# Kernel tuning notes

Measured on AMD Instinct MI355X. Metric: run time of the kernel, lower is better.

Reference implementation:

```python
import jax, jax.numpy as jnp
import numpy as np

N, E, B, D, H, L = 50000, 800000, 16, 64, 128, 2


def _lin(h, w, b):
    return h @ w + b


def _scatter_mean(v, idx, n):
    s = jax.ops.segment_sum(v, idx, num_segments=n)
    c = jax.ops.segment_sum(jnp.ones((v.shape[0],), v.dtype), idx, num_segments=n)
    return s / jnp.maximum(c, 1.0)[:, None]


def setup_inputs() -> dict:
    key = jax.random.key(0)
    ks = iter(jax.random.split(key, 40))

    def p(*shape):
        return jax.random.normal(next(ks), shape, dtype=jnp.float32) * 0.05

    inp = {
        "x": jax.random.normal(next(ks), (N, D), dtype=jnp.float32),
        "edge_attr": jax.random.normal(next(ks), (E, D), dtype=jnp.float32),
        "u": jax.random.normal(next(ks), (B, D), dtype=jnp.float32),
        "e_w1": p(L, 4 * D, H), "e_b1": p(L, H),
        "e_w2": p(L, H, H), "e_b2": p(L, H),
        "e_w3": p(L, H, D), "e_b3": p(L, D),
        "n1_w1": p(L, 2 * D, H), "n1_b1": p(L, H),
        "n1_w2": p(L, H, H), "n1_b2": p(L, H),
        "n2_w1": p(L, D + H + D, H), "n2_b1": p(L, H),
        "n2_w2": p(L, H, D), "n2_b2": p(L, D),
        "g_w1": p(L, 3 * D, H), "g_b1": p(L, H),
        "g_w2": p(L, H, D), "g_b2": p(L, D),
        "edge_index": jax.random.randint(next(ks), (2, E), 0, N, dtype=jnp.int32),
        "batch": jnp.sort(jax.random.randint(next(ks), (N,), 0, B, dtype=jnp.int32)),
    }
    return inp


def _forward(x, edge_attr, u, params, edge_index, batch):
    row, col = edge_index[0], edge_index[1]
    eb = batch[row]  # [E] graph id per edge
    x0, e0, u0 = x, edge_attr, u
    for l in range(L):
        (e_w1, e_b1, e_w2, e_b2, e_w3, e_b3,
         n1_w1, n1_b1, n1_w2, n1_b2,
         n2_w1, n2_b1, n2_w2, n2_b2,
         g_w1, g_b1, g_w2, g_b2) = [pm[l] for pm in params]
        # Edge model: [E, e+2n+u] -> MLP -> [E, D]
        h = jnp.concatenate([x[row], x[col], edge_attr, u[eb]], axis=1)
        h = jax.nn.relu(_lin(h, e_w1, e_b1))
        h = jax.nn.relu(_lin(h, e_w2, e_b2))
        edge_attr = _lin(h, e_w3, e_b3)
        # Node model: gather src node + edge, MLP1, scatter_mean onto dest, MLP2
        se = jnp.concatenate([x[row], edge_attr], axis=1)  # [E, 2D]
        se = _lin(jax.nn.relu(_lin(se, n1_w1, n1_b1)), n1_w2, n1_b2)
        agg = _scatter_mean(se, col, N)  # [N, H]
        xh = jnp.concatenate([x, agg, u[batch]], axis=1)
        x = _lin(jax.nn.relu(_lin(xh, n2_w1, n2_b1)), n2_w2, n2_b2)
        # Global model: per-graph means of updated nodes/edges
        e_agg = _scatter_mean(edge_attr, eb, B)
        n_agg = _scatter_mean(x, batch, B)
        uh = jnp.concatenate([u, n_agg, e_agg], axis=1)
        u = _lin(jax.nn.relu(_lin(uh, g_w1, g_b1)), g_w2, g_b2)
    return x + x0, edge_attr + e0, u + u0


def reference(x, edge_attr, u, e_w1, e_b1, e_w2, e_b2, e_w3, e_b3, n1_w1, n1_b1, n1_w2, n1_b2, n2_w1, n2_b1, n2_w2, n2_b2, g_w1, g_b1, g_w2, g_b2, edge_index, batch):
    params = (e_w1, e_b1, e_w2, e_b2, e_w3, e_b3,
              n1_w1, n1_b1, n1_w2, n1_b2,
              n2_w1, n2_b1, n2_w2, n2_b2,
              g_w1, g_b1, g_w2, g_b2)
    return _forward(x, edge_attr, u, params, edge_index, batch)
```

## Files before the change

kernel.cpp:

```cpp
#include <hip/hip_runtime.h>

#define N_NODES 50000
#define E_EDGES 800000
#define NG 16
#define DD 64
#define HH 128
#define NB_SCAN 49

typedef __attribute__((ext_vector_type(8))) __bf16 bf16x8;
typedef __attribute__((ext_vector_type(4))) float f32x4;
typedef unsigned int uint;
typedef unsigned short ushort;
typedef __attribute__((ext_vector_type(4))) uint uint4v;

#define MFMA16(a,b,c) __builtin_amdgcn_mfma_f32_16x16x32_bf16((a),(b),(c),0,0,0)

__device__ __forceinline__ ushort f2bf(float f){
  uint u = __builtin_bit_cast(uint, f);
  u += 0x7fffu + ((u >> 16) & 1u);
  return (ushort)(u >> 16);
}
__device__ __forceinline__ uint pk2(float a, float b){
  return (uint)f2bf(a) | ((uint)f2bf(b) << 16);
}
__device__ __forceinline__ float bflo(uint u){ return __builtin_bit_cast(float, u << 16); }
__device__ __forceinline__ float bfhi(uint u){ return __builtin_bit_cast(float, u & 0xffff0000u); }

__device__ __forceinline__ void bar(){
  asm volatile("s_waitcnt lgkmcnt(0)" ::: "memory");
  __builtin_amdgcn_s_barrier();
}
#define VMWAIT(n) asm volatile("s_waitcnt vmcnt(" #n ")" ::: "memory")

__device__ __forceinline__ void gload16(const void* g, void* l){
  __builtin_amdgcn_global_load_lds(
      (const __attribute__((address_space(1))) unsigned int*)g,
      (__attribute__((address_space(3))) unsigned int*)l, 16, 0, 0);
}

__device__ __forceinline__ bf16x8 ldfrag(const char* base, int row, int byteoff){
  uint4v v = *(const uint4v*)(base + row*256 + (byteoff ^ ((row & 7) << 4)));
  return __builtin_bit_cast(bf16x8, v);
}
__device__ __forceinline__ uint4v ld_chunk(const char* base, int row, int c16){
  return *(const uint4v*)(base + row*256 + ((c16*16) ^ ((row & 7) << 4)));
}
__device__ __forceinline__ void st_h(char* base, int row, int col, float v){
  *(ushort*)(base + row*256 + ((col*2) ^ ((row & 7) << 4))) = f2bf(v);
}
__device__ __forceinline__ void st_chunk(char* base, int row, int c16, uint4v v){
  *(uint4v*)(base + row*256 + ((c16*16) ^ ((row & 7) << 4))) = v;
}
__device__ __forceinline__ bf16x8 ldfrag128(const char* base, int row, int byteoff){
  uint4v v = *(const uint4v*)(base + row*128 + (byteoff ^ ((row & 7) << 4)));
  return __builtin_bit_cast(bf16x8, v);
}
__device__ __forceinline__ void st_chunk128(char* base, int row, int c16, uint4v v){
  *(uint4v*)(base + row*128 + ((c16*16) ^ ((row & 7) << 4))) = v;
}
__device__ __forceinline__ void pack16_128(char* dst, int r, int c16, const float* src){
  float4 lo = *(const float4*)src;
  float4 hi = *(const float4*)(src + 4);
  uint4v v; v.x = pk2(lo.x, lo.y); v.y = pk2(lo.z, lo.w);
  v.z = pk2(hi.x, hi.y); v.w = pk2(hi.z, hi.w);
  st_chunk128(dst, r, c16, v);
}

__device__ __forceinline__ void stage_b(char* sB, const ushort* wt,
                                        int Nout, int Ktot, int koff, int t, int stride){
  for (int task = t; task < Nout*16; task += stride){
    int n = task >> 4, c = task & 15;
    uint4v v = *(const uint4v*)(wt + (long)n*Ktot + koff + c*8);
    st_chunk(sB, n, c, v);
  }
}
template<int NT>
__device__ __forceinline__ void gemm_acc(const char* A, const char* B,
                                         int wv, int l15, int lhi, f32x4* acc){
  #pragma unroll
  for (int kt = 0; kt < 4; ++kt){
    bf16x8 a = ldfrag(A, wv*16 + l15, kt*64 + lhi*16);
    #pragma unroll
    for (int n = 0; n < NT; ++n){
      bf16x8 bb = ldfrag(B, n*16 + l15, kt*64 + lhi*16);
      acc[n] = MFMA16(a, bb, acc[n]);
    }
  }
}
template<int NT, bool RELU>
__device__ __forceinline__ void epi_lds(char* dst, const f32x4* acc, const float* bias,
                                        int wv, int l15, int lhi){
  #pragma unroll
  for (int n = 0; n < NT; ++n){
    float bv = bias[n*16 + l15];
    #pragma unroll
    for (int j = 0; j < 4; ++j){
      int r = wv*16 + lhi*4 + j;
      float v = acc[n][j] + bv;
      if (RELU) v = fmaxf(v, 0.f);
      st_h(dst, r, n*16 + l15, v);
    }
  }
}

__global__ void pack_weights(const float* __restrict__ e1, const float* __restrict__ e2,
                             const float* __restrict__ e3, const float* __restrict__ n12,
                             const float* __restrict__ n21, const float* __restrict__ n22,
                             ushort* __restrict__ out){
  int idx = blockIdx.x * 256 + threadIdx.x;
  int l = idx / 114688, r = idx % 114688;
  const float* src; int K, N, off;
  if      (r <  32768){ src = e1;  K = 256; N = 128; off = 0; }
  else if (r <  49152){ src = e2;  K = 128; N = 128; off = 32768; }
  else if (r <  57344){ src = e3;  K = 128; N = 64;  off = 49152; }
  else if (r <  73728){ src = n12; K = 128; N = 128; off = 57344; }
  else if (r < 106496){ src = n21; K = 256; N = 128; off = 73728; }
  else                { src = n22; K = 128; N = 64;  off = 106496; }
  int q = r - off; int k = q / N; int n = q % N;
  out[(long)l*139264 + off + n*K + k] = f2bf(src[(long)l*K*N + q]);
}

__global__ void make_wc(const float* __restrict__ n1w1, const float* __restrict__ ew3,
                        const float* __restrict__ n1b1, const float* __restrict__ eb3,
                        ushort* __restrict__ packed, float* __restrict__ biasc){
  int l = blockIdx.x, t = threadIdx.x;
  const float* W1 = n1w1 + (long)l*128*128;
  const float* W3 = ew3 + (long)l*128*64;
  ushort* wc = packed + (long)l*139264 + 114688;
  for (int i = t; i < 8192; i += 256){
    int k = i >> 7, n = i & 127;
    wc[n*192 + k] = f2bf(W1[k*128 + n]);
  }
  for (int i = t; i < 16384; i += 256){
    int k2 = i >> 7, n = i & 127;
    float s = 0.f;
    for (int m = 0; m < 64; ++m) s += W3[k2*64 + m] * W1[(64 + m)*128 + n];
    wc[n*192 + 64 + k2] = f2bf(s);
  }
  if (t < 128){
    float s = n1b1[l*128 + t];
    for (int m = 0; m < 64; ++m) s += eb3[l*64 + m] * W1[(64 + m)*128 + t];
    biasc[l*128 + t] = s;
  }
}

__global__ void hist_kernel(const int* __restrict__ edge_index, const int* __restrict__ batch,
                            int* __restrict__ deg, float* __restrict__ cnt_eb){
  __shared__ float h[NG];
  int t = threadIdx.x;
  if (t < NG) h[t] = 0.f;
  __syncthreads();
  int e = blockIdx.x * 256 + t;
  if (e < E_EDGES){
    atomicAdd(deg + edge_index[E_EDGES + e], 1);
    atomicAdd(&h[batch[edge_index[e]]], 1.f);
  }
  __syncthreads();
  if (t < NG) atomicAdd(cnt_eb + t, h[t]);
}
__global__ void count_nodes_kernel(const int* __restrict__ batch, float* __restrict__ cnt_b){
  __shared__ float h[NG];
  int t = threadIdx.x;
  if (t < NG) h[t] = 0.f;
  __syncthreads();
  int n = blockIdx.x * 256 + t;
  if (n < N_NODES) atomicAdd(&h[batch[n]], 1.f);
  __syncthreads();
  if (t < NG) atomicAdd(cnt_b + t, h[t]);
}
__global__ void scan_a(const int* __restrict__ deg, int* __restrict__ bsum){
  __shared__ int red[1024];
  int i = blockIdx.x*1024 + threadIdx.x;
  red[threadIdx.x] = (i < N_NODES) ? deg[i] : 0;
  __syncthreads();
  for (int s = 512; s > 0; s >>= 1){
    if ((int)threadIdx.x < s) red[threadIdx.x] += red[threadIdx.x + s];
    __syncthreads();
  }
  if (threadIdx.x == 0) bsum[blockIdx.x] = red[0];
}
__global__ void scan_b(const int* __restrict__ bsum, int* __restrict__ bbase){
  if (threadIdx.x == 0){
    int run = 0;
    for (int b = 0; b < NB_SCAN; ++b){ int v = bsum[b]; bbase[b] = run; run += v; }
  }
}
__global__ void scan_c(const int* __restrict__ deg, const int* __restrict__ bbase,
                       int* __restrict__ off, int* __restrict__ cursor){
  __shared__ int sc[1024];
  int i = blockIdx.x*1024 + threadIdx.x;
  int v = (i < N_NODES) ? deg[i] : 0;
  sc[threadIdx.x] = v;
  __syncthreads();
  for (int d = 1; d < 1024; d <<= 1){
    int add = ((int)threadIdx.x >= d) ? sc[threadIdx.x - d] : 0;
    __syncthreads();
    sc[threadIdx.x] += add;
    __syncthreads();
  }
  if (i < N_NODES){
    int ex = sc[threadIdx.x] - v + bbase[blockIdx.x];
    off[i] = ex; cursor[i] = ex;
  }
}
__global__ void fill_kernel(const int* __restrict__ edge_index, int* __restrict__ cursor,
                            int* __restrict__ pos){
  int e = blockIdx.x*256 + threadIdx.x;
  if (e < E_EDGES){
    int c = edge_index[E_EDGES + e];
    pos[e] = atomicAdd(&cursor[c], 1);
  }
}

__global__ __launch_bounds__(256, 3) void k123_kernel(
    const float* __restrict__ x_cur, const float* e_cur,
    const float* __restrict__ u_cur,
    const int* __restrict__ ei, const int* __restrict__ batch,
    const ushort* __restrict__ w1t, const ushort* __restrict__ w2t,
    const float* __restrict__ be1, const float* __restrict__ be2,
    ushort* h2g)
{
  __shared__ __align__(16) char lds[49152];
  __shared__ int sRow[128], sCol[128], sEb[128];
  char* A  = lds;
  char* B  = lds + 16384;
  char* OV = lds + 16384;
  const int t = threadIdx.x;
  const int wv = t >> 6, l15 = t & 15, lhi = (t >> 4) & 3;
  const int ebase = blockIdx.x * 128;

  if (t < 128){
    int r = ei[ebase + t];
    sRow[t] = r; sCol[t] = ei[E_EDGES + ebase + t]; sEb[t] = batch[r];
  }
  __syncthreads();

  f32x4 acc[2][8];
  #pragma unroll
  for (int m = 0; m < 2; ++m)
    #pragma unroll
    for (int n = 0; n < 8; ++n) acc[m][n] = f32x4{0,0,0,0};

  for (int c = 0; c < 4; ++c){
    #pragma unroll
    for (int it = 0; it < 4; ++it){
      int task = t + it*256, r = task >> 3, c16 = task & 7;
      const float* s;
      if      (c == 0) s = x_cur + (long)sRow[r]*DD + c16*8;
      else if (c == 1) s = x_cur + (long)sCol[r]*DD + c16*8;
      else if (c == 2) s = e_cur + (long)(ebase + r)*DD + c16*8;
      else             s = u_cur + (long)sEb[r]*DD + c16*8;
      pack16_128(A, r, c16, s);
    }
    #pragma unroll
    for (int it = 0; it < 4; ++it){
      int task = t + it*256, n = task >> 3, c16 = task & 7;
      st_chunk128(B, n, c16, *(const uint4v*)(w1t + (long)n*256 + c*64 + c16*8));
    }
    __syncthreads();
    #pragma unroll
    for (int kt = 0; kt < 2; ++kt){
      bf16x8 a0 = ldfrag128(A, wv*32 + l15,      kt*64 + lhi*16);
      bf16x8 a1 = ldfrag128(A, wv*32 + 16 + l15, kt*64 + lhi*16);
      #pragma unroll
      for (int n = 0; n < 8; ++n){
        bf16x8 bb = ldfrag128(B, n*16 + l15, kt*64 + lhi*16);
        acc[0][n] = MFMA16(a0, bb, acc[0][n]);
        acc[1][n] = MFMA16(a1, bb, acc[1][n]);
      }
    }
    __syncthreads();
  }
  #pragma unroll
  for (int m = 0; m < 2; ++m)
    #pragma unroll
    for (int n = 0; n < 8; ++n){
      int col = n*16 + l15;
      float bv = be1[col];
      #pragma unroll
      for (int j = 0; j < 4; ++j)
        st_h(OV, wv*32 + m*16 + lhi*4 + j, col, fmaxf(acc[m][n][j] + bv, 0.f));
    }
  __syncthreads();

  #pragma unroll
  for (int m = 0; m < 2; ++m)
    #pragma unroll
    for (int n = 0; n < 8; ++n) acc[m][n] = f32x4{0,0,0,0};
  for (int kc = 0; kc < 2; ++kc){
    #pragma unroll
    for (int it = 0; it < 4; ++it){
      int task = t + it*256, n = task >> 3, c16 = task & 7;
      st_chunk128(A, n, c16, *(const uint4v*)(w2t + (long)n*128 + kc*64 + c16*8));
    }
    __syncthreads();
    #pragma unroll
    for (int kt = 0; kt < 2; ++kt){
      bf16x8 a0 = ldfrag(OV, wv*32 + l15,      kc*128 + kt*64 + lhi*16);
      bf16x8 a1 = ldfrag(OV, wv*32 + 16 + l15, kc*128 + kt*64 + lhi*16);
      #pragma unroll
      for (int n = 0; n < 8; ++n){
        bf16x8 bb = ldfrag128(A, n*16 + l15, kt*64 + lhi*16);
        acc[0][n] = MFMA16(a0, bb, acc[0][n]);
        acc[1][n] = MFMA16(a1, bb, acc[1][n]);
      }
    }
    __syncthreads();
  }
  #pragma unroll
  for (int m = 0; m < 2; ++m)
    #pragma unroll
    for (int n = 0; n < 8; ++n){
      int col = n*16 + l15;
      float bv = be2[col];
      #pragma unroll
      for (int j = 0; j < 4; ++j)
        st_h(OV, wv*32 + m*16 + lhi*4 + j, col, fmaxf(acc[m][n][j] + bv, 0.f));
    }
  __syncthreads();
  #pragma unroll
  for (int it = 0; it < 8; ++it){
    int task = t + it*256, r = task >> 4, c16 = task & 15;
    *(uint4v*)(h2g + (long)(ebase + r)*HH + c16*8) = ld_chunk(OV, r, c16);
  }
}

template<bool CSR>
__global__ __launch_bounds__(256, 2) void k45_kernel(
    const float* __restrict__ x_cur, const ushort* h2g,
    const int* __restrict__ ei, const int* __restrict__ batch,
    const int* __restrict__ pos_arr,
    const ushort* __restrict__ w3t, const ushort* __restrict__ wct,
    const ushort* __restrict__ w5t,
    const float* __restrict__ be3, const float* __restrict__ biasc,
    const float* __restrict__ bn12,
    float* e_outf, const float* __restrict__ e_resid,
    ushort* __restrict__ se_buf, float* __restrict__ agg_sum,
    float* __restrict__ e_agg, int has_resid)
{
  __shared__ __align__(16) char lds[65536];
  __shared__ float sEagg[NG*DD];
  __shared__ int sRow[128];
  __shared__ int sDst[128];
  char* S0 = lds;
  char* S1 = lds + 16384;
  char* S2 = lds + 32768;
  char* S3 = lds + 49152;
  char* OV = lds;
  char* SE = lds + 32768;
  const int t = threadIdx.x;
  const int wv = t >> 6, lane = t & 63, l15 = t & 15, lhi = (t >> 4) & 3;
  const int ebase = blockIdx.x * 128;

  auto GL = [&](const ushort* base, long stride, int koff, char* slot){
    #pragma unroll
    for (int it = 0; it < 4; ++it){
      int q = (wv*4 + it)*64 + lane;
      int r = q >> 3, cp = q & 7;
      gload16(base + (long)r*stride + koff + ((cp ^ (r & 7))*8),
              slot + (wv*4 + it)*1024);
    }
  };

  if (t < 128){
    int r = ei[ebase + t];
    sDst[t] = CSR ? pos_arr[ebase + t] : ei[E_EDGES + ebase + t];
    sRow[t] = r | (batch[r] << 16);
  }
  GL(wct, 192, 0, S1);
  GL(h2g + (long)ebase*HH, HH, 0, S2);
  GL(wct, 192, 64, S3);
  bf16x8 b3[4][4];
  #pragma unroll
  for (int n = 0; n < 4; ++n)
    #pragma unroll
    for (int kk = 0; kk < 4; ++kk)
      b3[n][kk] = *(const bf16x8*)(w3t + (long)(n*16 + l15)*128 + kk*32 + lhi*8);
  for (int i = t; i < NG*DD; i += 256) sEagg[i] = 0.f;
  __syncthreads();

  #pragma unroll
  for (int it = 0; it < 4; ++it){
    int task = t + it*256, r = task >> 3, c16 = task & 7;
    pack16_128(S0, r, c16, x_cur + (long)(sRow[r] & 0xffff)*DD + c16*8);
  }
  __syncthreads();

  f32x4 acc4[2][8], acc3[2][4];
  #pragma unroll
  for (int m = 0; m < 2; ++m){
    #pragma unroll
    for (int n = 0; n < 8; ++n) acc4[m][n] = f32x4{0,0,0,0};
    #pragma unroll
    for (int n = 0; n < 4; ++n) acc3[m][n] = f32x4{0,0,0,0};
  }

  auto MM = [&](const char* A, const char* B){
    #pragma unroll
    for (int kt = 0; kt < 2; ++kt){
      bf16x8 a0 = ldfrag128(A, wv*32 + l15,      kt*64 + lhi*16);
      bf16x8 a1 = ldfrag128(A, wv*32 + 16 + l15, kt*64 + lhi*16);
      #pragma unroll
      for (int n = 0; n < 8; ++n){
        bf16x8 bb = ldfrag128(B, n*16 + l15, kt*64 + lhi*16);
        acc4[0][n] = MFMA16(a0, bb, acc4[0][n]);
        acc4[1][n] = MFMA16(a1, bb, acc4[1][n]);
      }
    }
  };
  auto MM3 = [&](const char* A, const char* B, int kkbase){
    #pragma unroll
    for (int kt = 0; kt < 2; ++kt){
      bf16x8 a0 = ldfrag128(A, wv*32 + l15,      kt*64 + lhi*16);
      bf16x8 a1 = ldfrag128(A, wv*32 + 16 + l15, kt*64 + lhi*16);
      #pragma unroll
      for (int n = 0; n < 8; ++n){
        bf16x8 bb = ldfrag128(B, n*16 + l15, kt*64 + lhi*16);
        acc4[0][n] = MFMA16(a0, bb, acc4[0][n]);
        acc4[1][n] = MFMA16(a1, bb, acc4[1][n]);
      }
      #pragma unroll
      for (int n = 0; n < 4; ++n){
        acc3[0][n] = MFMA16(a0, b3[n][kkbase + kt], acc3[0][n]);
        acc3[1][n] = MFMA16(a1, b3[n][kkbase + kt], acc3[1][n]);
      }
    }
  };

  MM(S0, S1);
  bar();
  GL(h2g + (long)ebase*HH, HH, 64, S0);
  GL(wct, 192, 128, S1);
  MM3(S2, S3, 0);
  bar();
  GL(w5t, 128, 0, S2);
  VMWAIT(4);
  __builtin_amdgcn_s_barrier();
  MM3(S0, S1, 2);
  bar();
  #pragma unroll
  for (int m = 0; m < 2; ++m)
    #pragma unroll
    for (int n = 0; n < 8; ++n){
      int col = n*16 + l15;
      float bv = biasc[col];
      #pragma unroll
      for (int j = 0; j < 4; ++j)
        st_h(OV, wv*32 + m*16 + lhi*4 + j, col, fmaxf(acc4[m][n][j] + bv, 0.f));
    }
  GL(w5t, 128, 64, S3);
  VMWAIT(4);
  bar();
  f32x4 acc5[2][8];
  #pragma unroll
  for (int m = 0; m < 2; ++m)
    #pragma unroll
    for (int n = 0; n < 8; ++n) acc5[m][n] = f32x4{0,0,0,0};
  #pragma unroll
  for (int kt = 0; kt < 2; ++kt){
    bf16x8 a0 = ldfrag(OV, wv*32 + l15,      kt*64 + lhi*16);
    bf16x8 a1 = ldfrag(OV, wv*32 + 16 + l15, kt*64 + lhi*16);
    #pragma unroll
    for (int n = 0; n < 8; ++n){
      bf16x8 bb = ldfrag128(S2, n*16 + l15, kt*64 + lhi*16);
      acc5[0][n] = MFMA16(a0, bb, acc5[0][n]);
      acc5[1][n] = MFMA16(a1, bb, acc5[1][n]);
    }
  }
  VMWAIT(0);
  __builtin_amdgcn_s_barrier();
  #pragma unroll
  for (int kt = 0; kt < 2; ++kt){
    bf16x8 a0 = ldfrag(OV, wv*32 + l15,      128 + kt*64 + lhi*16);
    bf16x8 a1 = ldfrag(OV, wv*32 + 16 + l15, 128 + kt*64 + lhi*16);
    #pragma unroll
    for (int n = 0; n < 8; ++n){
      bf16x8 bb = ldfrag128(S3, n*16 + l15, kt*64 + lhi*16);
      acc5[0][n] = MFMA16(a0, bb, acc5[0][n]);
      acc5[1][n] = MFMA16(a1, bb, acc5[1][n]);
    }
  }
  bar();

  #pragma unroll
  for (int m = 0; m < 2; ++m)
    #pragma unroll
    for (int n = 0; n < 4; ++n){
      int col = n*16 + l15;
      float bv = be3[col];
      #pragma unroll
      for (int j = 0; j < 4; ++j){
        int row = wv*32 + m*16 + lhi*4 + j;
        float v = acc3[m][n][j] + bv;
        long eg = (long)(ebase + row)*DD + col;
        e_outf[eg] = has_resid ? (v + e_resid[eg]) : v;
        atomicAdd(&sEagg[(sRow[row] >> 16)*DD + col], v);
      }
    }
  if (CSR){
    #pragma unroll
    for (int m = 0; m < 2; ++m)
      #pragma unroll
      for (int n = 0; n < 8; ++n){
        int col = n*16 + l15;
        float bv = bn12[col];
        #pragma unroll
        for (int j = 0; j < 4; ++j)
          st_h(SE, wv*32 + m*16 + lhi*4 + j, col, acc5[m][n][j] + bv);
      }
    bar();
    #pragma unroll
    for (int it = 0; it < 8; ++it){
      int task = t + it*256, r = task >> 4, c16 = task & 15;
      *(uint4v*)(se_buf + (long)sDst[r]*HH + c16*8) = ld_chunk(SE, r, c16);
    }
  } else {
    #pragma unroll
    for (int m = 0; m < 2; ++m)
      #pragma unroll
      for (int n = 0; n < 8; ++n){
        int col = n*16 + l15;
        float bv = bn12[col];
        #pragma unroll
        for (int j = 0; j < 4; ++j){
          int row = wv*32 + m*16 + lhi*4 + j;
          atomicAdd(agg_sum + (long)sDst[row]*HH + col, acc5[m][n][j] + bv);
        }
      }
    bar();
  }
  for (int i = t; i < NG*DD; i += 256) atomicAdd(e_agg + i, sEagg[i]);
}

template<bool CSR>
__global__ __launch_bounds__(256, 2) void node_kernel(
    const float* __restrict__ x_cur, const float* __restrict__ u_cur,
    const float* __restrict__ x_resid, const int* __restrict__ batch,
    const ushort* __restrict__ se_buf, const int* __restrict__ deg,
    const int* __restrict__ off, const float* __restrict__ agg_sum,
    const ushort* __restrict__ w_n21, const ushort* __restrict__ w_n22,
    const float* __restrict__ b_n21, const float* __restrict__ b_n22,
    float* __restrict__ x_out, float* __restrict__ n_agg, int has_resid)
{
  __shared__ __align__(16) char sA[16384];
  __shared__ __align__(16) char sB[32768];
  __shared__ __align__(16) char sH[16384];
  __shared__ int sBat[64], sDeg[64], sOff[64];
  __shared__ float sRinv[64];
  __shared__ float sNagg[NG*DD];

  const int t = threadIdx.x;
  const int wv = t >> 6, ln = t & 63, l15 = ln & 15, lhi = ln >> 4;
  const int n0 = blockIdx.x * 64;

  if (t < 64){
    int nd = n0 + t;
    int ok = nd < N_NODES;
    sBat[t] = ok ? batch[nd] : 0;
    int d = ok ? deg[nd] : 0;
    sDeg[t] = d;
    sOff[t] = ok ? off[nd] : 0;
    sRinv[t] = 1.f / fmaxf((float)d, 1.f);
  }
  for (int i = t; i < NG*DD; i += 256) sNagg[i] = 0.f;
  __syncthreads();

  float s[32];
  const int r4 = t >> 2, q = t & 3;
  if (CSR){
    #pragma unroll
    for (int k = 0; k < 32; ++k) s[k] = 0.f;
    int d = sDeg[r4], o = sOff[r4];
    for (int i = 0; i < d; ++i){
      const ushort* src = se_buf + (long)(o + i)*HH + q*32;
      #pragma unroll
      for (int c = 0; c < 4; ++c){
        uint4v v = *(const uint4v*)(src + c*8);
        #pragma unroll
        for (int jj = 0; jj < 4; ++jj){
          s[c*8 + jj*2]     += bflo(v[jj]);
          s[c*8 + jj*2 + 1] += bfhi(v[jj]);
        }
      }
    }
    float riv = sRinv[r4];
    #pragma unroll
    for (int k = 0; k < 32; ++k) s[k] *= riv;
  }

  f32x4 acc[8];
  #pragma unroll
  for (int n = 0; n < 8; ++n) acc[n] = f32x4{0.f,0.f,0.f,0.f};

  for (int half = 0; half < 2; ++half){
    if (CSR){
      for (int task = t; task < 512; task += 256){
        int r = task >> 3, c = task & 7;
        int nd = n0 + r;
        bool ok = nd < N_NODES;
        float4 lo = {0,0,0,0}, hi = {0,0,0,0};
        if (ok){
          const float* src = (half == 0) ? (x_cur + (long)nd*DD + c*8)
                                         : (u_cur + (long)sBat[r]*DD + c*8);
          lo = *(const float4*)src; hi = *(const float4*)(src + 4);
        }
        uint4v v; v.x = pk2(lo.x, lo.y); v.y = pk2(lo.z, lo.w);
        v.z = pk2(hi.x, hi.y); v.w = pk2(hi.z, hi.w);
        st_chunk(sA, r, (half == 0) ? c : (8 + c), v);
      }
      if ((half == 0 && q < 2) || (half == 1 && q >= 2)){
        int cbase = (half == 0) ? (8 + q*4) : ((q - 2)*4);
        #pragma unroll
        for (int cc = 0; cc < 4; ++cc){
          uint4v v;
          v.x = pk2(s[cc*8+0], s[cc*8+1]); v.y = pk2(s[cc*8+2], s[cc*8+3]);
          v.z = pk2(s[cc*8+4], s[cc*8+5]); v.w = pk2(s[cc*8+6], s[cc*8+7]);
          st_chunk(sA, r4, cbase + cc, v);
        }
      }
    } else {
      for (int task = t; task < 1024; task += 256){
        int r = task >> 4, c = task & 15;
        int nd = n0 + r;
        bool ok = nd < N_NODES;
        float scale = 1.f;
        const float* src;
        if (half == 0){
          if (c < 8) src = x_cur + (long)nd*DD + c*8;
          else { src = agg_sum + (long)nd*HH + (c-8)*8; scale = sRinv[r]; }
        } else {
          if (c < 8){ src = agg_sum + (long)nd*HH + 64 + c*8; scale = sRinv[r]; }
          else src = u_cur + (long)sBat[r]*DD + (c-8)*8;
        }
        float4 lo = {0,0,0,0}, hi = {0,0,0,0};
        if (ok){ lo = *(const float4*)src; hi = *(const float4*)(src + 4); }
        uint4v v; v.x = pk2(lo.x*scale, lo.y*scale); v.y = pk2(lo.z*scale, lo.w*scale);
        v.z = pk2(hi.x*scale, hi.y*scale); v.w = pk2(hi.z*scale, hi.w*scale);
        st_chunk(sA, r, c, v);
      }
    }
    stage_b(sB, w_n21, 128, 256, half*128, t, 256);
    __syncthreads();
    gemm_acc<8>(sA, sB, wv, l15, lhi, acc);
    __syncthreads();
  }
  epi_lds<8, true>(sH, acc, b_n21, wv, l15, lhi);
  stage_b(sB, w_n22, 64, 128, 0, t, 256);
  __syncthreads();

  f32x4 acc2[4];
  #pragma unroll
  for (int n = 0; n < 4; ++n) acc2[n] = f32x4{0.f,0.f,0.f,0.f};
  gemm_acc<4>(sH, sB, wv, l15, lhi, acc2);

  #pragma unroll
  for (int n = 0; n < 4; ++n){
    float bv = b_n22[n*16 + l15];
    #pragma unroll
    for (int j = 0; j < 4; ++j){
      int r = wv*16 + lhi*4 + j;
      int nd = n0 + r;
      if (nd < N_NODES){
        int col = n*16 + l15;
        float v = acc2[n][j] + bv;
        long xg = (long)nd*DD + col;
        x_out[xg] = has_resid ? (v + x_resid[xg]) : v;
        atomicAdd(&sNagg[sBat[r]*DD + col], v);
      }
    }
  }
  __syncthreads();
  for (int i = t; i < NG*DD; i += 256) atomicAdd(n_agg + i, sNagg[i]);
}

__global__ void global_kernel(const float* __restrict__ u_cur, const float* __restrict__ n_agg,
                              const float* __restrict__ e_agg, const float* __restrict__ cnt_b,
                              const float* __restrict__ cnt_e,
                              const float* __restrict__ g_w1, const float* __restrict__ g_b1,
                              const float* __restrict__ g_w2, const float* __restrict__ g_b2,
                              const float* __restrict__ u_resid, float* __restrict__ u_out,
                              int has_resid)
{
  int g = blockIdx.x, t = threadIdx.x;
  __shared__ float uh[192];
  __shared__ float hb[128];
  float v;
  if (t < 64)       v = u_cur[g*64 + t];
  else if (t < 128) v = n_agg[g*64 + (t-64)] / fmaxf(cnt_b[g], 1.f);
  else              v = e_agg[g*64 + (t-128)] / fmaxf(cnt_e[g], 1.f);
  uh[t] = v;
  __syncthreads();
  if (t < 128){
    float s = g_b1[t];
    for (int k = 0; k < 192; ++k) s += uh[k] * g_w1[k*128 + t];
    hb[t] = fmaxf(s, 0.f);
  }
  __syncthreads();
  if (t < 64){
    float s = g_b2[t];
    for (int k = 0; k < 128; ++k) s += hb[k] * g_w2[k*64 + t];
    if (has_resid) s += u_resid[g*64 + t];
    u_out[g*64 + t] = s;
  }
}

extern "C" void kernel_launch(void* const* d_in, const int* in_sizes, int n_in,
                              void* d_out, int out_size, void* d_ws, size_t ws_size,
                              hipStream_t stream)
{
  const float* x0   = (const float*)d_in[0];
  const float* e0   = (const float*)d_in[1];
  const float* u0   = (const float*)d_in[2];
  const float* e_w1 = (const float*)d_in[3];
  const float* e_b1 = (const float*)d_in[4];
  const float* e_w2 = (const float*)d_in[5];
  const float* e_b2 = (const float*)d_in[6];
  const float* e_w3 = (const float*)d_in[7];
  const float* e_b3 = (const float*)d_in[8];
  const float* n1_w1 = (const float*)d_in[9];
  const float* n1_b1 = (const float*)d_in[10];
  const float* n1_w2 = (const float*)d_in[11];
  const float* n1_b2 = (const float*)d_in[12];
  const float* n2_w1 = (const float*)d_in[13];
  const float* n2_b1 = (const float*)d_in[14];
  const float* n2_w2 = (const float*)d_in[15];
  const float* n2_b2 = (const float*)d_in[16];
  const float* g_w1 = (const float*)d_in[17];
  const float* g_b1 = (const float*)d_in[18];
  const float* g_w2 = (const float*)d_in[19];
  const float* g_b2 = (const float*)d_in[20];
  const int* edge_index = (const int*)d_in[21];
  const int* batch      = (const int*)d_in[22];

  float* out_x = (float*)d_out;
  float* out_e = out_x + (long)N_NODES*DD;
  float* out_u = out_e + (long)E_EDGES*DD;

  char* ws = (char*)d_ws;
  int*   deg    = (int*)(ws + 0);
  int*   off    = (int*)(ws + 200000);
  int*   cursor = (int*)(ws + 400000);
  int*   bsum   = (int*)(ws + 600000);
  int*   bbase  = (int*)(ws + 600256);
  float* cnt_eb = (float*)(ws + 600512);
  float* cnt_b  = (float*)(ws + 600576);
  float* e_agg  = (float*)(ws + 600640);
  float* n_agg  = (float*)(ws + 604736);
  float* biascf = (float*)(ws + 608832);
  ushort* packed = (ushort*)(ws + 609856);
  const size_t big = 1166912;
  bool use_csr = ws_size >= (size_t)(big + 204800000 + 3200000);
  ushort* se_buf = (ushort*)(ws + big);
  int*    pos    = (int*)(ws + big + 204800000);
  float*  agg_sum = (float*)(ws + big);

  (void)hipMemsetAsync(deg, 0, 200000, stream);
  (void)hipMemsetAsync(cnt_eb, 0, 128, stream);
  pack_weights<<<896, 256, 0, stream>>>(e_w1, e_w2, e_w3, n1_w2, n2_w1, n2_w2, packed);
  make_wc<<<2, 256, 0, stream>>>(n1_w1, e_w3, n1_b1, e_b3, packed, biascf);
  hist_kernel<<<3125, 256, 0, stream>>>(edge_index, batch, deg, cnt_eb);
  count_nodes_kernel<<<196, 256, 0, stream>>>(batch, cnt_b);
  if (use_csr){
    scan_a<<<NB_SCAN, 1024, 0, stream>>>(deg, bsum);
    scan_b<<<1, 64, 0, stream>>>(bsum, bbase);
    scan_c<<<NB_SCAN, 1024, 0, stream>>>(deg, bbase, off, cursor);
    fill_kernel<<<3125, 256, 0, stream>>>(edge_index, cursor, pos);
  }

  const float* xc = x0;
  const float* ec = e0;
  const float* uc = u0;
  for (int l = 0; l < 2; ++l){
    (void)hipMemsetAsync(e_agg, 0, 8192, stream);
    if (!use_csr)
      (void)hipMemsetAsync(agg_sum, 0, (size_t)N_NODES*HH*4, stream);
    const ushort* P = packed + (long)l*139264;
    k123_kernel<<<6250, 256, 0, stream>>>(
        xc, ec, uc, edge_index, batch,
        P + 0, P + 32768, e_b1 + l*128, e_b2 + l*128,
        (ushort*)out_e);
    if (use_csr){
      k45_kernel<true><<<6250, 256, 0, stream>>>(
          xc, (const ushort*)out_e, edge_index, batch, pos,
          P + 49152, P + 114688, P + 57344,
          e_b3 + l*64, biascf + l*128, n1_b2 + l*128,
          out_e, e0, se_buf, agg_sum, e_agg, l == 1);
      node_kernel<true><<<782, 256, 0, stream>>>(
          xc, uc, x0, batch, se_buf, deg, off, agg_sum,
          P + 73728, P + 106496, n2_b1 + l*128, n2_b2 + l*64,
          out_x, n_agg, l == 1);
    } else {
      k45_kernel<false><<<6250, 256, 0, stream>>>(
          xc, (const ushort*)out_e, edge_index, batch, pos,
          P + 49152, P + 114688, P + 57344,
          e_b3 + l*64, biascf + l*128, n1_b2 + l*128,
          out_e, e0, se_buf, agg_sum, e_agg, l == 1);
      node_kernel<false><<<782, 256, 0, stream>>>(
          xc, uc, x0, batch, se_buf, deg, off, agg_sum,
          P + 73728, P + 106496, n2_b1 + l*128, n2_b2 + l*64,
          out_x, n_agg, l == 1);
    }
    global_kernel<<<NG, 192, 0, stream>>>(
        uc, n_agg, e_agg, cnt_b, cnt_eb,
        g_w1 + l*192*128, g_b1 + l*128, g_w2 + l*128*64, g_b2 + l*64,
        u0, out_u, l == 1);
    xc = out_x; ec = out_e; uc = out_u;
  }
}
```

Baseline: 1.794 ms.

## Shrink k45 LDS to three slots for higher occupancy and replicate edge aggregates

Cuts the k45 kernel's shared staging buffer from four 16KB slots to three by reusing S1 and S2 for later weight tiles. The SE staging for the scatter output now reuses OV, and launch bounds rise to three blocks per CU. Bias values are preloaded into registers. Per-graph edge-aggregate atomics are spread across 32 replicas indexed by block, which global_kernel sums, to reduce global atomic contention. The slot reuse adds extra barriers and serialized load waits, and register pressure may spill under the tighter launch bound.

```diff
diff --git a/kernel.cpp b/kernel.cpp
--- a/kernel.cpp
+++ b/kernel.cpp
@@ -6,6 +6,7 @@
 #define DD 64
 #define HH 128
 #define NB_SCAN 49
+#define EREP 32
 
 typedef __attribute__((ext_vector_type(8))) __bf16 bf16x8;
 typedef __attribute__((ext_vector_type(4))) float f32x4;
@@ -326,7 +327,7 @@
 }
 
 template<bool CSR>
-__global__ __launch_bounds__(256, 2) void k45_kernel(
+__global__ __launch_bounds__(256, 3) void k45_kernel(
     const float* __restrict__ x_cur, const ushort* h2g,
     const int* __restrict__ ei, const int* __restrict__ batch,
     const int* __restrict__ pos_arr,
@@ -336,18 +337,16 @@
     const float* __restrict__ bn12,
     float* e_outf, const float* __restrict__ e_resid,
     ushort* __restrict__ se_buf, float* __restrict__ agg_sum,
-    float* __restrict__ e_agg, int has_resid)
+    float* __restrict__ e_agg_rep, int has_resid)
 {
-  __shared__ __align__(16) char lds[65536];
+  __shared__ __align__(16) char lds[49152];
   __shared__ float sEagg[NG*DD];
   __shared__ int sRow[128];
   __shared__ int sDst[128];
   char* S0 = lds;
   char* S1 = lds + 16384;
   char* S2 = lds + 32768;
-  char* S3 = lds + 49152;
   char* OV = lds;
-  char* SE = lds + 32768;
   const int t = threadIdx.x;
   const int wv = t >> 6, lane = t & 63, l15 = t & 15, lhi = (t >> 4) & 3;
   const int ebase = blockIdx.x * 128;
@@ -369,13 +368,17 @@
   }
   GL(wct, 192, 0, S1);
   GL(h2g + (long)ebase*HH, HH, 0, S2);
-  GL(wct, 192, 64, S3);
   bf16x8 b3[4][4];
   #pragma unroll
   for (int n = 0; n < 4; ++n)
     #pragma unroll
     for (int kk = 0; kk < 4; ++kk)
       b3[n][kk] = *(const bf16x8*)(w3t + (long)(n*16 + l15)*128 + kk*32 + lhi*8);
+  float bvc[8], bv5[8], bv3[4];
+  #pragma unroll
+  for (int n = 0; n < 8; ++n){ bvc[n] = biasc[n*16 + l15]; bv5[n] = bn12[n*16 + l15]; }
+  #pragma unroll
+  for (int n = 0; n < 4; ++n) bv3[n] = be3[n*16 + l15];
   for (int i = t; i < NG*DD; i += 256) sEagg[i] = 0.f;
   __syncthreads();
 
@@ -394,7 +397,6 @@
     #pragma unroll
     for (int n = 0; n < 4; ++n) acc3[m][n] = f32x4{0,0,0,0};
   }
-
   auto MM = [&](const char* A, const char* B){
     #pragma unroll
     for (int kt = 0; kt < 2; ++kt){
@@ -429,10 +431,13 @@
 
   MM(S0, S1);
   bar();
+  GL(wct, 192, 64, S1);
   GL(h2g + (long)ebase*HH, HH, 64, S0);
+  VMWAIT(4);
+  __builtin_amdgcn_s_barrier();
+  MM3(S2, S1, 0);
+  bar();
   GL(wct, 192, 128, S1);
-  MM3(S2, S3, 0);
-  bar();
   GL(w5t, 128, 0, S2);
   VMWAIT(4);
   __builtin_amdgcn_s_barrier();
@@ -443,13 +448,11 @@
     #pragma unroll
     for (int n = 0; n < 8; ++n){
       int col = n*16 + l15;
-      float bv = biasc[col];
       #pragma unroll
       for (int j = 0; j < 4; ++j)
-        st_h(OV, wv*32 + m*16 + lhi*4 + j, col, fmaxf(acc4[m][n][j] + bv, 0.f));
-    }
-  GL(w5t, 128, 64, S3);
-  VMWAIT(4);
+        st_h(OV, wv*32 + m*16 + lhi*4 + j, col, fmaxf(acc4[m][n][j] + bvc[n], 0.f));
+    }
+  VMWAIT(0);
   bar();
   f32x4 acc5[2][8];
   #pragma unroll
@@ -467,6 +470,8 @@
       acc5[1][n] = MFMA16(a1, bb, acc5[1][n]);
     }
   }
+  bar();
+  GL(w5t, 128, 64, S2);
   VMWAIT(0);
   __builtin_amdgcn_s_barrier();
   #pragma unroll
@@ -475,61 +480,59 @@
     bf16x8 a1 = ldfrag(OV, wv*32 + 16 + l15, 128 + kt*64 + lhi*16);
     #pragma unroll
     for (int n = 0; n < 8; ++n){
-      bf16x8 bb = ldfrag128(S3, n*16 + l15, kt*64 + lhi*16);
+      bf16x8 bb = ldfrag128(S2, n*16 + l15, kt*64 + lhi*16);
       acc5[0][n] = MFMA16(a0, bb, acc5[0][n]);
       acc5[1][n] = MFMA16(a1, bb, acc5[1][n]);
     }
   }
   bar();
 
+  if (CSR){
+    #pragma unroll
+    for (int m = 0; m < 2; ++m)
+      #pragma unroll
+      for (int n = 0; n < 8; ++n){
+        int col = n*16 + l15;
+        #pragma unroll
+        for (int j = 0; j < 4; ++j)
+          st_h(OV, wv*32 + m*16 + lhi*4 + j, col, acc5[m][n][j] + bv5[n]);
+      }
+    bar();
+    #pragma unroll
+    for (int it = 0; it < 8; ++it){
+      int task = t + it*256, r = task >> 4, c16 = task & 15;
+      *(uint4v*)(se_buf + (long)sDst[r]*HH + c16*8) = ld_chunk(OV, r, c16);
+    }
+  } else {
+    #pragma unroll
+    for (int m = 0; m < 2; ++m)
+      #pragma unroll
+      for (int n = 0; n < 8; ++n){
+        int col = n*16 + l15;
+        #pragma unroll
+        for (int j = 0; j < 4; ++j){
+          int row = wv*32 + m*16 + lhi*4 + j;
+          atomicAdd(agg_sum + (long)sDst[row]*HH + col, acc5[m][n][j] + bv5[n]);
+        }
+      }
+  }
   #pragma unroll
   for (int m = 0; m < 2; ++m)
     #pragma unroll
     for (int n = 0; n < 4; ++n){
       int col = n*16 + l15;
-      float bv = be3[col];
       #pragma unroll
       for (int j = 0; j < 4; ++j){
         int row = wv*32 + m*16 + lhi*4 + j;
-        float v = acc3[m][n][j] + bv;
+        float v = acc3[m][n][j] + bv3[n];
         long eg = (long)(ebase + row)*DD + col;
         e_outf[eg] = has_resid ? (v + e_resid[eg]) : v;
         atomicAdd(&sEagg[(sRow[row] >> 16)*DD + col], v);
       }
     }
-  if (CSR){
-    #pragma unroll
-    for (int m = 0; m < 2; ++m)
-      #pragma unroll
-      for (int n = 0; n < 8; ++n){
-        int col = n*16 + l15;
-        float bv = bn12[col];
-        #pragma unroll
-        for (int j = 0; j < 4; ++j)
-          st_h(SE, wv*32 + m*16 + lhi*4 + j, col, acc5[m][n][j] + bv);
-      }
-    bar();
-    #pragma unroll
-    for (int it = 0; it < 8; ++it){
-      int task = t + it*256, r = task >> 4, c16 = task & 15;
-      *(uint4v*)(se_buf + (long)sDst[r]*HH + c16*8) = ld_chunk(SE, r, c16);
-    }
-  } else {
-    #pragma unroll
-    for (int m = 0; m < 2; ++m)
-      #pragma unroll
-      for (int n = 0; n < 8; ++n){
-        int col = n*16 + l15;
-        float bv = bn12[col];
-        #pragma unroll
-        for (int j = 0; j < 4; ++j){
-          int row = wv*32 + m*16 + lhi*4 + j;
-          atomicAdd(agg_sum + (long)sDst[row]*HH + col, acc5[m][n][j] + bv);
-        }
-      }
-    bar();
-  }
-  for (int i = t; i < NG*DD; i += 256) atomicAdd(e_agg + i, sEagg[i]);
+  __syncthreads();
+  float* dst = e_agg_rep + (long)(blockIdx.x & (EREP - 1))*NG*DD;
+  for (int i = t; i < NG*DD; i += 256) atomicAdd(dst + i, sEagg[i]);
 }
 
 template<bool CSR>
@@ -674,7 +677,7 @@
 }
 
 __global__ void global_kernel(const float* __restrict__ u_cur, const float* __restrict__ n_agg,
-                              const float* __restrict__ e_agg, const float* __restrict__ cnt_b,
+                              const float* __restrict__ e_agg_rep, const float* __restrict__ cnt_b,
                               const float* __restrict__ cnt_e,
                               const float* __restrict__ g_w1, const float* __restrict__ g_b1,
                               const float* __restrict__ g_w2, const float* __restrict__ g_b2,
@@ -687,7 +690,11 @@
   float v;
   if (t < 64)       v = u_cur[g*64 + t];
   else if (t < 128) v = n_agg[g*64 + (t-64)] / fmaxf(cnt_b[g], 1.f);
-  else              v = e_agg[g*64 + (t-128)] / fmaxf(cnt_e[g], 1.f);
+  else {
+    float s = 0.f;
+    for (int c = 0; c < EREP; ++c) s += e_agg_rep[c*NG*DD + g*64 + (t-128)];
+    v = s / fmaxf(cnt_e[g], 1.f);
+  }
   uh[t] = v;
   __syncthreads();
   if (t < 128){
@@ -744,11 +751,11 @@
   int*   bbase  = (int*)(ws + 600256);
   float* cnt_eb = (float*)(ws + 600512);
   float* cnt_b  = (float*)(ws + 600576);
-  float* e_agg  = (float*)(ws + 600640);
   float* n_agg  = (float*)(ws + 604736);
   float* biascf = (float*)(ws + 608832);
   ushort* packed = (ushort*)(ws + 609856);
-  const size_t big = 1166912;
+  float* e_agg_rep = (float*)(ws + 1166912);
+  const size_t big = 1297984;
   bool use_csr = ws_size >= (size_t)(big + 204800000 + 3200000);
   ushort* se_buf = (ushort*)(ws + big);
   int*    pos    = (int*)(ws + big + 204800000);
@@ -771,7 +778,8 @@
   const float* ec = e0;
   const float* uc = u0;
   for (int l = 0; l < 2; ++l){
-    (void)hipMemsetAsync(e_agg, 0, 8192, stream);
+    (void)hipMemsetAsync(n_agg, 0, 4096, stream);
+    (void)hipMemsetAsync(e_agg_rep, 0, EREP*NG*DD*4, stream);
     if (!use_csr)
       (void)hipMemsetAsync(agg_sum, 0, (size_t)N_NODES*HH*4, stream);
     const ushort* P = packed + (long)l*139264;
@@ -784,7 +792,7 @@
           xc, (const ushort*)out_e, edge_index, batch, pos,
           P + 49152, P + 114688, P + 57344,
           e_b3 + l*64, biascf + l*128, n1_b2 + l*128,
-          out_e, e0, se_buf, agg_sum, e_agg, l == 1);
+          out_e, e0, se_buf, agg_sum, e_agg_rep, l == 1);
       node_kernel<true><<<782, 256, 0, stream>>>(
           xc, uc, x0, batch, se_buf, deg, off, agg_sum,
           P + 73728, P + 106496, n2_b1 + l*128, n2_b2 + l*64,
@@ -794,14 +802,14 @@
           xc, (const ushort*)out_e, edge_index, batch, pos,
           P + 49152, P + 114688, P + 57344,
           e_b3 + l*64, biascf + l*128, n1_b2 + l*128,
-          out_e, e0, se_buf, agg_sum, e_agg, l == 1);
+          out_e, e0, se_buf, agg_sum, e_agg_rep, l == 1);
       node_kernel<false><<<782, 256, 0, stream>>>(
           xc, uc, x0, batch, se_buf, deg, off, agg_sum,
           P + 73728, P + 106496, n2_b1 + l*128, n2_b2 + l*64,
           out_x, n_agg, l == 1);
     }
     global_kernel<<<NG, 192, 0, stream>>>(
-        uc, n_agg, e_agg, cnt_b, cnt_eb,
+        uc, n_agg, e_agg_rep, cnt_b, cnt_eb,
         g_w1 + l*192*128, g_b1 + l*128, g_w2 + l*128*64, g_b2 + l*64,
         u0, out_u, l == 1);
     xc = out_x; ec = out_e; uc = out_u;
```

Measured after the change: 2.402 ms. 33.9% more time.
